# Performance work log

Hardware: AMD Instinct MI355X
Metric: run time of the kernel (lower is better)

Reference implementation:

```python
import jax, jax.numpy as jnp
import numpy as np

G, C, L, D, H, NCLS = 64, 32, 128, 64, 128, 10


def setup_inputs() -> dict:
    key = jax.random.key(0)
    ks = jax.random.split(key, 5)
    scale = 0.05
    return {
        "cycle_reps": jax.random.normal(ks[0], (G, C, L, D), dtype=jnp.float32),
        "W_ih": jax.random.normal(ks[1], (4 * H, D), dtype=jnp.float32) * scale,
        "W_hh": jax.random.normal(ks[2], (4 * H, H), dtype=jnp.float32) * scale,
        "b_ih": jnp.zeros((4 * H,), dtype=jnp.float32),
        "b_hh": jnp.zeros((4 * H,), dtype=jnp.float32),
        "W_cls": jax.random.normal(ks[3], (NCLS, H), dtype=jnp.float32) * scale,
        "b_cls": jnp.zeros((NCLS,), dtype=jnp.float32),
    }


def _lstm_seq_sum(x, W_ih, W_hh, b):
    """Run a single-layer LSTM over x [B, L, D]; return sum of hidden states over L -> [B, H]."""
    B = x.shape[0]
    Hh = W_hh.shape[1]
    # precompute input-side gate pre-activations for all timesteps: [L, B, 4H]
    xg = jnp.einsum('bld,gd->lbg', x, W_ih) + b

    def step(carry, xg_t):
        h, c = carry
        gates = xg_t + h @ W_hh.T  # [B, 4H]
        i, f, g, o = jnp.split(gates, 4, axis=-1)  # torch i/f/g/o gate order
        i = jax.nn.sigmoid(i)
        f = jax.nn.sigmoid(f)
        g = jnp.tanh(g)
        o = jax.nn.sigmoid(o)
        c = f * c + i * g
        h = o * jnp.tanh(c)
        return (h, c), h

    init = (jnp.zeros((B, Hh), x.dtype), jnp.zeros((B, Hh), x.dtype))
    _, hs = jax.lax.scan(step, init, xg)  # hs: [L, B, H]
    return hs.sum(axis=0)


def reference(cycle_reps, W_ih, W_hh, b_ih, b_hh, W_cls, b_cls):
    Gn, Cn, Ln, Dn = cycle_reps.shape
    x = cycle_reps.reshape(Gn * Cn, Ln, Dn)
    rep = _lstm_seq_sum(x, W_ih, W_hh, b_ih + b_hh)  # [G*C, H]: sum of LSTM outputs over seq
    rep = rep.reshape(Gn, Cn, -1)
    # torch.var_mean over the cycle axis; only the mean is used as the graph rep
    graph_mean = rep.mean(axis=1)  # [G, H]
    logits = graph_mean @ W_cls.T + b_cls  # classifier_gnn
    return jax.nn.log_softmax(logits, axis=1)
```

## Files before the change

kernel.cpp:

```cpp
#include <hip/hip_runtime.h>
#include <hip/hip_bf16.h>

#define NSEQ 2048
#define LSEQ 128
#define DIN  64
#define HID  128
#define NCLS 10
#define XPAD 72
#define HPAD 136
#define CHK  16

typedef __attribute__((ext_vector_type(8))) short bfrag8;
typedef __attribute__((ext_vector_type(4))) float facc4;

__device__ __forceinline__ short f2bf(float f) {
    union { __hip_bfloat16 b; short s; } u;
    u.b = __float2bfloat16(f);
    return u.s;
}

__device__ __forceinline__ bfrag8 load_bf16_frag(const float* __restrict__ p) {
    bfrag8 r;
#pragma unroll
    for (int j = 0; j < 8; ++j) r[j] = f2bf(p[j]);
    return r;
}

__device__ __forceinline__ float fast_sigmoid(float x) {
    float e = __builtin_amdgcn_exp2f(-1.4426950408889634f * x);
    return __builtin_amdgcn_rcpf(1.0f + e);
}
__device__ __forceinline__ float fast_tanh(float x) {
    float e = __builtin_amdgcn_exp2f(2.8853900817779268f * x);
    return 1.0f - 2.0f * __builtin_amdgcn_rcpf(1.0f + e);
}

__global__ __launch_bounds__(512) void lstm_fused(
    const float* __restrict__ x,
    const float* __restrict__ Wih,
    const float* __restrict__ Whh,
    const float* __restrict__ bih,
    const float* __restrict__ bhh,
    float* __restrict__ rep)
{
    __shared__ __align__(16) __hip_bfloat16 hbuf[2][8][HPAD];
    __shared__ __align__(16) __hip_bfloat16 xs[2][CHK][8][XPAD];

    const int tid  = threadIdx.x;
    const int w    = tid >> 6;
    const int lane = tid & 63;
    const int ln   = lane & 15;
    const int qd   = lane >> 4;
    const int s0   = blockIdx.x * 8;
    const int khid = w * 16 + ln;
    const int arow = ln >> 1;
    const int sq0  = 2 * qd;
    const int sq1  = 2 * qd + 1;

    bfrag8 whh[4][4];
    bfrag8 wih[4][2];
    facc4  biasf[4];
#pragma unroll
    for (int g = 0; g < 4; ++g) {
        const int col = g * HID + khid;
        const float b = bih[col] + bhh[col];
        biasf[g] = (facc4){b, b, b, b};
#pragma unroll
        for (int k0 = 0; k0 < 4; ++k0)
            whh[g][k0] = load_bf16_frag(Whh + col * HID + k0 * 32 + qd * 8);
#pragma unroll
        for (int k0 = 0; k0 < 2; ++k0)
            wih[g][k0] = load_bf16_frag(Wih + col * DIN + k0 * 32 + qd * 8);
    }

    {
        unsigned int* p = (unsigned int*)&hbuf[0][0][0];
        for (int i = tid; i < 2 * 8 * HPAD / 2; i += 512) p[i] = 0u;
    }

    const float* xsrc = x + (size_t)(s0 + w) * (LSEQ * DIN) + lane * 16;
    const int stt = lane >> 2;
    const int sdd = (lane & 3) * 16;

    {
        float4 a0 = ((const float4*)xsrc)[0];
        float4 a1 = ((const float4*)xsrc)[1];
        float4 a2 = ((const float4*)xsrc)[2];
        float4 a3 = ((const float4*)xsrc)[3];
        bfrag8 o0, o1;
#pragma unroll
        for (int j = 0; j < 4; ++j) { o0[j] = f2bf(((float*)&a0)[j]); o0[4+j] = f2bf(((float*)&a1)[j]); }
#pragma unroll
        for (int j = 0; j < 4; ++j) { o1[j] = f2bf(((float*)&a2)[j]); o1[4+j] = f2bf(((float*)&a3)[j]); }
        *(bfrag8*)&xs[0][stt][w][sdd]     = o0;
        *(bfrag8*)&xs[0][stt][w][sdd + 8] = o1;
    }

    float cst[2]  = {0.f, 0.f};
    float hsum[2] = {0.f, 0.f};

    __syncthreads();

    facc4 accA[4], accB[4];
    {
        bfrag8 x0 = *(const bfrag8*)(&xs[0][0][arow][qd * 8]);
        bfrag8 x1 = *(const bfrag8*)(&xs[0][0][arow][32 + qd * 8]);
#pragma unroll
        for (int g = 0; g < 4; ++g) {
            accA[g] = __builtin_amdgcn_mfma_f32_16x16x32_bf16(x0, wih[g][0], biasf[g], 0, 0, 0);
            accA[g] = __builtin_amdgcn_mfma_f32_16x16x32_bf16(x1, wih[g][1], accA[g], 0, 0, 0);
        }
    }

    int cur = 0;

#define STEP(ACCIN, ACCOUT, CT, XF)                                                      \
    {                                                                                    \
        const int ct = (CT);                                                             \
        const int nbuf = (ct < CHK - 1) ? buf : (buf ^ 1);                               \
        const int nct  = (ct + 1) & (CHK - 1);                                           \
        bfrag8 hf[4];                                                                    \
        bfrag8 xf0, xf1;                                                                 \
        if (XF) {                                                                        \
                            \
            xf0 = *(const bfrag8*)(&xs[nbuf][nct][arow][qd * 8]);                        \
            xf1 = *(const bfrag8*)(&xs[nbuf][nct][arow][32 + qd * 8]);                   \
            _Pragma("unroll")                                                            \
            for (int g = 0; g < 4; ++g) {                                                \
                ACCOUT[g] = __builtin_amdgcn_mfma_f32_16x16x32_bf16(xf0, wih[g][0], biasf[g], 0, 0, 0); \
                ACCOUT[g] = __builtin_amdgcn_mfma_f32_16x16x32_bf16(xf1, wih[g][1], ACCOUT[g], 0, 0, 0); \
            }                                                                            \
            _Pragma("unroll")                                                            \
            for (int k0 = 0; k0 < 4; ++k0)                                               \
                hf[k0] = *(const bfrag8*)(&hbuf[cur][arow][k0 * 32 + qd * 8]);           \
        } else {                                                                         \
            _Pragma("unroll")                                                            \
            for (int k0 = 0; k0 < 4; ++k0)                                               \
                hf[k0] = *(const bfrag8*)(&hbuf[cur][arow][k0 * 32 + qd * 8]);           \
            xf0 = *(const bfrag8*)(&xs[nbuf][nct][arow][qd * 8]);                        \
            xf1 = *(const bfrag8*)(&xs[nbuf][nct][arow][32 + qd * 8]);                   \
        }                                                                                \
                    \
        _Pragma("unroll")                                                                \
        for (int g = 0; g < 4; ++g)                                                      \
            _Pragma("unroll")                                                            \
            for (int k0 = 0; k0 < 4; ++k0)                                               \
                ACCIN[g] = __builtin_amdgcn_mfma_f32_16x16x32_bf16(hf[k0], whh[g][k0], ACCIN[g], 0, 0, 0); \
                     \
        float u0[4], u1[4];                                                              \
        _Pragma("unroll")                                                                \
        for (int g = 0; g < 4; ++g) { u0[g] = ACCIN[g][0]; u1[g] = ACCIN[g][2]; }        \
        if (!XF) {                                                                       \
                              \
            _Pragma("unroll")                                                            \
            for (int g = 0; g < 4; ++g) {                                                \
                ACCOUT[g] = __builtin_amdgcn_mfma_f32_16x16x32_bf16(xf0, wih[g][0], biasf[g], 0, 0, 0); \
                ACCOUT[g] = __builtin_amdgcn_mfma_f32_16x16x32_bf16(xf1, wih[g][1], ACCOUT[g], 0, 0, 0); \
            }                                                                            \
        }                                                                                \
        if (ct == 0 && more) {                      \
            const float* p = xsrc + (chunk + 1) * (CHK * DIN);                           \
            l0 = ((const float4*)p)[0];                                                  \
            l1 = ((const float4*)p)[1];                                                  \
            l2 = ((const float4*)p)[2];                                                  \
            l3 = ((const float4*)p)[3];                                                  \
        }                                                                                \
        if (ct == 12 && more) {                   \
            bfrag8 o0, o1;                                                               \
            _Pragma("unroll")                                                            \
            for (int j = 0; j < 4; ++j) { o0[j] = f2bf(((float*)&l0)[j]); o0[4+j] = f2bf(((float*)&l1)[j]); } \
            _Pragma("unroll")                                                            \
            for (int j = 0; j < 4; ++j) { o1[j] = f2bf(((float*)&l2)[j]); o1[4+j] = f2bf(((float*)&l3)[j]); } \
            *(bfrag8*)&xs[buf ^ 1][stt][w][sdd]     = o0;                                \
            *(bfrag8*)&xs[buf ^ 1][stt][w][sdd + 8] = o1;                                \
        }                                                                                \
                         \
        short hb[2];                                                                     \
        _Pragma("unroll")                                                                \
        for (int j = 0; j < 2; ++j) {                                                    \
            float iv = fast_sigmoid(j ? u1[0] : u0[0]);                                  \
            float fv = fast_sigmoid(j ? u1[1] : u0[1]);                                  \
            float gv = fast_tanh(j ? u1[2] : u0[2]);                                     \
            float ov = fast_sigmoid(j ? u1[3] : u0[3]);                                  \
            float c  = fv * cst[j] + iv * gv;                                            \
            cst[j]   = c;                                                                \
            float hv = ov * fast_tanh(c);                                                \
            hsum[j] += hv;                                                               \
            hb[j]    = f2bf(hv);                                                         \
        }                                                                                \
        ((short*)&hbuf[cur ^ 1][sq0][0])[khid] = hb[0];                                  \
        ((short*)&hbuf[cur ^ 1][sq1][0])[khid] = hb[1];                                  \
        __syncthreads();                                                                 \
        cur ^= 1;                                                                        \
    }

    if (w < 4) {
        for (int chunk = 0; chunk < LSEQ / CHK; ++chunk) {
            const int buf = chunk & 1;
            const bool more = chunk < (LSEQ / CHK - 1);
            float4 l0, l1, l2, l3;
#pragma unroll 1
            for (int ct2 = 0; ct2 < CHK / 2; ++ct2) {
                STEP(accA, accB, 2 * ct2, 0);
                STEP(accB, accA, 2 * ct2 + 1, 0);
            }
        }
    } else {
        for (int chunk = 0; chunk < LSEQ / CHK; ++chunk) {
            const int buf = chunk & 1;
            const bool more = chunk < (LSEQ / CHK - 1);
            float4 l0, l1, l2, l3;
#pragma unroll 1
            for (int ct2 = 0; ct2 < CHK / 2; ++ct2) {
                STEP(accA, accB, 2 * ct2, 1);
                STEP(accB, accA, 2 * ct2 + 1, 1);
            }
        }
    }
#undef STEP

    rep[(size_t)(s0 + sq0) * HID + khid] = hsum[0];
    rep[(size_t)(s0 + sq1) * HID + khid] = hsum[1];
}

__global__ __launch_bounds__(128) void cls_kernel(
    const float* __restrict__ rep,
    const float* __restrict__ Wcls,
    const float* __restrict__ bcls,
    float* __restrict__ out)
{
    __shared__ float m_s[HID];
    __shared__ float logits_s[NCLS];
    const int g = blockIdx.x;
    const int h = threadIdx.x;

    float s = 0.f;
#pragma unroll 4
    for (int c = 0; c < 32; ++c)
        s += rep[((size_t)g * 32 + c) * HID + h];
    m_s[h] = s * (1.0f / 32.0f);
    __syncthreads();

    if (h < NCLS) {
        float acc = bcls[h];
        for (int k = 0; k < HID; ++k)
            acc += m_s[k] * Wcls[h * HID + k];
        logits_s[h] = acc;
    }
    __syncthreads();

    if (h < NCLS) {
        float mx = logits_s[0];
#pragma unroll
        for (int j = 1; j < NCLS; ++j) mx = fmaxf(mx, logits_s[j]);
        float se = 0.f;
#pragma unroll
        for (int j = 0; j < NCLS; ++j)
            se += __builtin_amdgcn_exp2f((logits_s[j] - mx) * 1.4426950408889634f);
        float lse = mx + 0.6931471805599453f * __builtin_amdgcn_logf(se);
        out[g * NCLS + h] = logits_s[h] - lse;
    }
}

extern "C" void kernel_launch(void* const* d_in, const int* in_sizes, int n_in,
                              void* d_out, int out_size, void* d_ws, size_t ws_size,
                              hipStream_t stream) {
    const float* x    = (const float*)d_in[0];
    const float* Wih  = (const float*)d_in[1];
    const float* Whh  = (const float*)d_in[2];
    const float* bih  = (const float*)d_in[3];
    const float* bhh  = (const float*)d_in[4];
    const float* Wcls = (const float*)d_in[5];
    const float* bcls = (const float*)d_in[6];

    float* rep = (float*)d_ws;

    lstm_fused<<<NSEQ / 8, 512, 0, stream>>>(x, Wih, Whh, bih, bhh, rep);
    cls_kernel<<<64, 128, 0, stream>>>(rep, Wcls, bcls, (float*)d_out);
}
```

Before: 190.9 us.

## Split hidden-state recurrence into two half-block waves with staggered barriers

The hidden vector is split into two halves held in separate LDS buffers. Waves 0-3 produce the first half and waves 4-7 the second half, offset by one half-step, so each half's gate nonlinearities overlap with MFMA work on the other half across two barriers per step. __syncthreads is replaced by a raw s_barrier preceded by an lgkmcnt wait, and the inner chunk loop is fully unrolled. This adds a second barrier per timestep and more complex phase bookkeeping, including a tail cell computation for the lagging group.

Result: slower. 202.6 us (+6.1%).

```diff
diff --git a/kernel.cpp b/kernel.cpp
--- a/kernel.cpp
+++ b/kernel.cpp
@@ -7,7 +7,7 @@
 #define HID  128
 #define NCLS 10
 #define XPAD 72
-#define HPAD 136
+#define HXP  72
 #define CHK  16
 
 typedef __attribute__((ext_vector_type(8))) short bfrag8;
@@ -33,6 +33,29 @@
 __device__ __forceinline__ float fast_tanh(float x) {
     float e = __builtin_amdgcn_exp2f(2.8853900817779268f * x);
     return 1.0f - 2.0f * __builtin_amdgcn_rcpf(1.0f + e);
+}
+
+__device__ __forceinline__ void block_barrier() {
+    asm volatile("s_waitcnt lgkmcnt(0)" ::: "memory");
+    __builtin_amdgcn_s_barrier();
+    asm volatile("" ::: "memory");
+}
+
+__device__ __forceinline__ void lstm_cell(const float u0[4], const float u1[4],
+                                          float cst[2], float hsum[2], short hb[2]) {
+#pragma unroll
+    for (int j = 0; j < 2; ++j) {
+        const float* u = j ? u1 : u0;
+        float iv = fast_sigmoid(u[0]);
+        float fv = fast_sigmoid(u[1]);
+        float gv = fast_tanh(u[2]);
+        float ov = fast_sigmoid(u[3]);
+        float c  = fv * cst[j] + iv * gv;
+        cst[j]   = c;
+        float hv = ov * fast_tanh(c);
+        hsum[j] += hv;
+        hb[j]    = f2bf(hv);
+    }
 }
 
 __global__ __launch_bounds__(512) void lstm_fused(
@@ -43,7 +66,8 @@
     const float* __restrict__ bhh,
     float* __restrict__ rep)
 {
-    __shared__ __align__(16) __hip_bfloat16 hbuf[2][8][HPAD];
+    __shared__ __align__(16) __hip_bfloat16 hbA[2][8][HXP];
+    __shared__ __align__(16) __hip_bfloat16 hbB[2][8][HXP];
     __shared__ __align__(16) __hip_bfloat16 xs[2][CHK][8][XPAD];
 
     const int tid  = threadIdx.x;
@@ -53,6 +77,7 @@
     const int qd   = lane >> 4;
     const int s0   = blockIdx.x * 8;
     const int khid = w * 16 + ln;
+    const int khb  = khid & 63;
     const int arow = ln >> 1;
     const int sq0  = 2 * qd;
     const int sq1  = 2 * qd + 1;
@@ -74,8 +99,10 @@
     }
 
     {
-        unsigned int* p = (unsigned int*)&hbuf[0][0][0];
-        for (int i = tid; i < 2 * 8 * HPAD / 2; i += 512) p[i] = 0u;
+        unsigned int* pa = (unsigned int*)&hbA[0][0][0];
+        for (int i = tid; i < 2 * 8 * HXP / 2; i += 512) pa[i] = 0u;
+        unsigned int* pb = (unsigned int*)&hbB[0][0][0];
+        for (int i = tid; i < 2 * 8 * HXP / 2; i += 512) pb[i] = 0u;
     }
 
     const float* xsrc = x + (size_t)(s0 + w) * (LSEQ * DIN) + lane * 16;
@@ -99,7 +126,7 @@
     float cst[2]  = {0.f, 0.f};
     float hsum[2] = {0.f, 0.f};
 
-    __syncthreads();
+    block_barrier();
 
     facc4 accA[4], accB[4];
     {
@@ -114,43 +141,33 @@
 
     int cur = 0;
 
-#define STEP(ACCIN, ACCOUT, CT, XF)                                                      \
+#define STEP(ACCIN, ACCOUT, CT, ISA, FIRST)                                              \
     {                                                                                    \
-        const int ct = (CT);                                                             \
+        const int ct   = (CT);                                                           \
         const int nbuf = (ct < CHK - 1) ? buf : (buf ^ 1);                               \
         const int nct  = (ct + 1) & (CHK - 1);                                           \
-        bfrag8 hf[4];                                                                    \
-        bfrag8 xf0, xf1;                                                                 \
-        if (XF) {                                                                        \
                             \
+        if (!ISA) {                  \
+            if (!(FIRST && chunk == 0)) {                                                \
+                float u0[4], u1[4];                                                      \
+                _Pragma("unroll")                                                        \
+                for (int g = 0; g < 4; ++g) { u0[g] = ACCOUT[g][0]; u1[g] = ACCOUT[g][2]; } \
+                short hb[2];                                                             \
+                lstm_cell(u0, u1, cst, hsum, hb);                                        \
+                ((short*)&hbB[cur][sq0][0])[khb] = hb[0];     \
+                ((short*)&hbB[cur][sq1][0])[khb] = hb[1];                                \
+            }                                                                            \
+        }                                                                                \
+        {                                                                                \
+            bfrag8 hfA0 = *(const bfrag8*)(&hbA[cur][arow][qd * 8]);                     \
+            bfrag8 hfA1 = *(const bfrag8*)(&hbA[cur][arow][32 + qd * 8]);                \
             xf0 = *(const bfrag8*)(&xs[nbuf][nct][arow][qd * 8]);                        \
             xf1 = *(const bfrag8*)(&xs[nbuf][nct][arow][32 + qd * 8]);                   \
             _Pragma("unroll")                                                            \
             for (int g = 0; g < 4; ++g) {                                                \
-                ACCOUT[g] = __builtin_amdgcn_mfma_f32_16x16x32_bf16(xf0, wih[g][0], biasf[g], 0, 0, 0); \
-                ACCOUT[g] = __builtin_amdgcn_mfma_f32_16x16x32_bf16(xf1, wih[g][1], ACCOUT[g], 0, 0, 0); \
+                ACCIN[g] = __builtin_amdgcn_mfma_f32_16x16x32_bf16(hfA0, whh[g][0], ACCIN[g], 0, 0, 0); \
+                ACCIN[g] = __builtin_amdgcn_mfma_f32_16x16x32_bf16(hfA1, whh[g][1], ACCIN[g], 0, 0, 0); \
             }                                                                            \
-            _Pragma("unroll")                                                            \
-            for (int k0 = 0; k0 < 4; ++k0)                                               \
-                hf[k0] = *(const bfrag8*)(&hbuf[cur][arow][k0 * 32 + qd * 8]);           \
-        } else {                                                                         \
-            _Pragma("unroll")                                                            \
-            for (int k0 = 0; k0 < 4; ++k0)                                               \
-                hf[k0] = *(const bfrag8*)(&hbuf[cur][arow][k0 * 32 + qd * 8]);           \
-            xf0 = *(const bfrag8*)(&xs[nbuf][nct][arow][qd * 8]);                        \
-            xf1 = *(const bfrag8*)(&xs[nbuf][nct][arow][32 + qd * 8]);                   \
-        }                                                                                \
-                    \
-        _Pragma("unroll")                                                                \
-        for (int g = 0; g < 4; ++g)                                                      \
-            _Pragma("unroll")                                                            \
-            for (int k0 = 0; k0 < 4; ++k0)                                               \
-                ACCIN[g] = __builtin_amdgcn_mfma_f32_16x16x32_bf16(hf[k0], whh[g][k0], ACCIN[g], 0, 0, 0); \
-                     \
-        float u0[4], u1[4];                                                              \
-        _Pragma("unroll")                                                                \
-        for (int g = 0; g < 4; ++g) { u0[g] = ACCIN[g][0]; u1[g] = ACCIN[g][2]; }        \
-        if (!XF) {                                                                       \
                               \
             _Pragma("unroll")                                                            \
             for (int g = 0; g < 4; ++g) {                                                \
@@ -165,6 +182,26 @@
             l2 = ((const float4*)p)[2];                                                  \
             l3 = ((const float4*)p)[3];                                                  \
         }                                                                                \
+        block_barrier();                                                                 \
+                          \
+        {                                                                                \
+            bfrag8 hfB0 = *(const bfrag8*)(&hbB[cur][arow][qd * 8]);                     \
+            bfrag8 hfB1 = *(const bfrag8*)(&hbB[cur][arow][32 + qd * 8]);                \
+            _Pragma("unroll")                                                            \
+            for (int g = 0; g < 4; ++g) {                                                \
+                ACCIN[g] = __builtin_amdgcn_mfma_f32_16x16x32_bf16(hfB0, whh[g][2], ACCIN[g], 0, 0, 0); \
+                ACCIN[g] = __builtin_amdgcn_mfma_f32_16x16x32_bf16(hfB1, whh[g][3], ACCIN[g], 0, 0, 0); \
+            }                                                                            \
+        }                                                                                \
+        if (ISA) {                   \
+            float u0[4], u1[4];                                                          \
+            _Pragma("unroll")                                                            \
+            for (int g = 0; g < 4; ++g) { u0[g] = ACCIN[g][0]; u1[g] = ACCIN[g][2]; }    \
+            short hb[2];                                                                 \
+            lstm_cell(u0, u1, cst, hsum, hb);                                            \
+            ((short*)&hbA[cur ^ 1][sq0][0])[khb] = hb[0];                                \
+            ((short*)&hbA[cur ^ 1][sq1][0])[khb] = hb[1];                                \
+        }                                                                                \
         if (ct == 12 && more) {                   \
             bfrag8 o0, o1;                                                               \
             _Pragma("unroll")                                                            \
@@ -174,47 +211,42 @@
             *(bfrag8*)&xs[buf ^ 1][stt][w][sdd]     = o0;                                \
             *(bfrag8*)&xs[buf ^ 1][stt][w][sdd + 8] = o1;                                \
         }                                                                                \
-                         \
-        short hb[2];                                                                     \
-        _Pragma("unroll")                                                                \
-        for (int j = 0; j < 2; ++j) {                                                    \
-            float iv = fast_sigmoid(j ? u1[0] : u0[0]);                                  \
-            float fv = fast_sigmoid(j ? u1[1] : u0[1]);                                  \
-            float gv = fast_tanh(j ? u1[2] : u0[2]);                                     \
-            float ov = fast_sigmoid(j ? u1[3] : u0[3]);                                  \
-            float c  = fv * cst[j] + iv * gv;                                            \
-            cst[j]   = c;                                                                \
-            float hv = ov * fast_tanh(c);                                                \
-            hsum[j] += hv;                                                               \
-            hb[j]    = f2bf(hv);                                                         \
-        }                                                                                \
-        ((short*)&hbuf[cur ^ 1][sq0][0])[khid] = hb[0];                                  \
-        ((short*)&hbuf[cur ^ 1][sq1][0])[khid] = hb[1];                                  \
-        __syncthreads();                                                                 \
+        block_barrier();                                                                 \
         cur ^= 1;                                                                        \
     }
 
     if (w < 4) {
+#pragma unroll 1
         for (int chunk = 0; chunk < LSEQ / CHK; ++chunk) {
             const int buf = chunk & 1;
             const bool more = chunk < (LSEQ / CHK - 1);
             float4 l0, l1, l2, l3;
-#pragma unroll 1
+            bfrag8 xf0, xf1;
+#pragma unroll
             for (int ct2 = 0; ct2 < CHK / 2; ++ct2) {
-                STEP(accA, accB, 2 * ct2, 0);
-                STEP(accB, accA, 2 * ct2 + 1, 0);
+                STEP(accA, accB, 2 * ct2,     1, (ct2 == 0));
+                STEP(accB, accA, 2 * ct2 + 1, 1, 0);
             }
         }
     } else {
+#pragma unroll 1
         for (int chunk = 0; chunk < LSEQ / CHK; ++chunk) {
             const int buf = chunk & 1;
             const bool more = chunk < (LSEQ / CHK - 1);
             float4 l0, l1, l2, l3;
-#pragma unroll 1
+            bfrag8 xf0, xf1;
+#pragma unroll
             for (int ct2 = 0; ct2 < CHK / 2; ++ct2) {
-                STEP(accA, accB, 2 * ct2, 1);
-                STEP(accB, accA, 2 * ct2 + 1, 1);
+                STEP(accA, accB, 2 * ct2,     0, (ct2 == 0));
+                STEP(accB, accA, 2 * ct2 + 1, 0, 0);
             }
+        }
+        {
+            float u0[4], u1[4];
+#pragma unroll
+            for (int g = 0; g < 4; ++g) { u0[g] = accB[g][0]; u1[g] = accB[g][2]; }
+            short hb[2];
+            lstm_cell(u0, u1, cst, hsum, hb);
         }
     }
 #undef STEP
```
